# Performance work log

Measured on AMD Instinct MI355X. Metric: run time of the kernel, lower is better.

The kernel has to match this reference:

```python
import jax, jax.numpy as jnp
import numpy as np


def _bucket_ids(x, min_t_idx, sz):
    # torch .long() truncates toward zero; x >= 0 so trunc == floor
    y = (x * sz).astype(jnp.int32)
    NI = x.shape[1]
    mt = min_t_idx.astype(jnp.int32)
    if NI == 2:
        return y[:, 0] * sz + y[:, 1] + mt * sz ** 2
    elif NI == 3:
        return y[:, 0] * sz ** 2 + y[:, 1] * sz + y[:, 2] + mt * sz ** 3
    else:
        raise AssertionError('Only 2D and 3D are supported')


def _max_bucket(x, min_t_idx, K, sz):
    # concrete (numpy) computation of the max bucket occupancy -> pad width M
    xn = np.asarray(x); mt = np.asarray(min_t_idx)
    msk = mt > 0
    y = (xn[msk] * sz).astype(np.int64)
    NI = xn.shape[1]
    if NI == 2:
        yf = y[:, 0] * sz + y[:, 1] + mt[msk].astype(np.int64) * sz ** 2
    else:
        yf = y[:, 0] * sz ** 2 + y[:, 1] * sz + y[:, 2] + mt[msk].astype(np.int64) * sz ** 3
    return max(int(np.bincount(yf).max()), K)


def _forward(x, min_t_idx, K, sz, M):
    N, NI = x.shape
    m = min_t_idx > 0
    y_f = _bucket_ids(x, min_t_idx, sz)
    # inactive points get unique singleton buckets sorted past all real ones
    BIG = jnp.int32(1 << 20)
    y_f = jnp.where(m, y_f, BIG + jnp.arange(N, dtype=jnp.int32))
    order = jnp.argsort(y_f)
    xs = x[order]              # [N, NI] sorted by bucket
    yfs = y_f[order]
    ms = m[order]
    # contiguous bucket extent for every point (block-diagonal ranges)
    left = jnp.searchsorted(yfs, yfs, side='left')
    count = jnp.searchsorted(yfs, yfs, side='right') - left
    # gather up-to-M in-bucket neighbors per point
    nb = jnp.arange(M)
    idx = jnp.clip(left[:, None] + nb[None, :], 0, N - 1)   # [N, M]
    nb_valid = nb[None, :] < count[:, None]                  # [N, M]
    xn = xs[idx]                                             # [N, M, NI]
    d2 = jnp.sum((xs[:, None, :] - xn) ** 2, axis=-1)        # [N, M]
    d2 = jnp.where(nb_valid, d2, jnp.inf)
    # K-th smallest squared distance in bucket (self included, dist 0) == argKmin[:, -1]
    kth = -jax.lax.top_k(-d2, K)[0][:, K - 1]
    w = jnp.sqrt(kth)
    dim = NI - 1
    if dim == 1:
        p_m = w * 2.0 / (K - 1)
    elif dim == 2:
        p_m = (w ** 2) * jnp.pi / (K - 1)
    else:
        p_m = (4.0 / 3.0) * (w ** 3) * jnp.pi / (K - 1)
    p_sorted = jnp.where(ms, p_m, 0.0)
    # scatter back to original ordering (p[m] = p_m[inv_sort_idx])
    return jnp.zeros(N, x.dtype).at[order].set(p_sorted)


def setup_inputs():
    key = jax.random.key(0)
    k1, k2 = jax.random.split(key)
    x = jax.random.uniform(k1, (262144, 3), dtype=jnp.float32)
    min_t_idx = jax.random.randint(k2, (262144,), 0, 32, dtype=jnp.int32)
    return {"x": x, "min_t_idx": min_t_idx, "K": 16, "sz": 5}


def reference(x, min_t_idx, K, sz):
    M = _max_bucket(x, min_t_idx, K, sz)
    return _forward(x, min_t_idx, K, sz, M)
```

## Files before the change

### kernel.cpp

```cpp
#include <hip/hip_runtime.h>
#include <math.h>

#define KK 16
#define NBUCK 4000
#define NBPAD 4096
#define CAP 128
#define INF_F __builtin_inff()

__global__ __launch_bounds__(256) void zero_kernel(int* __restrict__ counts) {
    int i = blockIdx.x * blockDim.x + threadIdx.x;
    if (i < NBPAD) counts[i] = 0;
}

__global__ __launch_bounds__(256) void build_kernel(const float4* __restrict__ xf4,
                                                    const int4* __restrict__ mt4,
                                                    int* __restrict__ counts,
                                                    float4* __restrict__ slab,
                                                    float* __restrict__ out, int N4) {
    int g = blockIdx.x * blockDim.x + threadIdx.x;
    if (g >= N4) return;
    float4 a = xf4[g * 3 + 0];
    float4 b = xf4[g * 3 + 1];
    float4 c = xf4[g * 3 + 2];
    int4 m = mt4[g];
    int i0 = g * 4;
    float px[4] = {a.x, a.w, b.z, c.y};
    float py[4] = {a.y, b.x, b.w, c.z};
    float pz[4] = {a.z, b.y, c.x, c.w};
    int   pm[4] = {m.x, m.y, m.z, m.w};
#pragma unroll
    for (int t = 0; t < 4; ++t) {
        int mm = pm[t];
        if (mm <= 0) { out[i0 + t] = 0.0f; continue; }
        float x0 = px[t], x1 = py[t], x2 = pz[t];
        int bid = mm * 125 + (int)(x0 * 5.0f) * 25 + (int)(x1 * 5.0f) * 5 + (int)(x2 * 5.0f);
        int pos = atomicAdd(&counts[bid], 1);
        if (pos < CAP)
            slab[(bid << 7) + pos] = make_float4(x0, x1, x2, __int_as_float(i0 + t));
    }
}

#define CAS(a, b) { float _lo = fminf(a, b); float _hi = fmaxf(a, b); a = _lo; b = _hi; }

#define SORT16_D \
  CAS(d0,d1) CAS(d2,d3) CAS(d4,d5) CAS(d6,d7) CAS(d8,d9) CAS(d10,d11) CAS(d12,d13) CAS(d14,d15) \
  CAS(d0,d2) CAS(d1,d3) CAS(d4,d6) CAS(d5,d7) CAS(d8,d10) CAS(d9,d11) CAS(d12,d14) CAS(d13,d15) \
  CAS(d1,d2) CAS(d5,d6) CAS(d9,d10) CAS(d13,d14) \
  CAS(d0,d4) CAS(d1,d5) CAS(d2,d6) CAS(d3,d7) CAS(d8,d12) CAS(d9,d13) CAS(d10,d14) CAS(d11,d15) \
  CAS(d2,d4) CAS(d3,d5) CAS(d10,d12) CAS(d11,d13) \
  CAS(d1,d2) CAS(d3,d4) CAS(d5,d6) CAS(d9,d10) CAS(d11,d12) CAS(d13,d14) \
  CAS(d0,d8) CAS(d1,d9) CAS(d2,d10) CAS(d3,d11) CAS(d4,d12) CAS(d5,d13) CAS(d6,d14) CAS(d7,d15) \
  CAS(d4,d8) CAS(d5,d9) CAS(d6,d10) CAS(d7,d11) \
  CAS(d2,d4) CAS(d3,d5) CAS(d6,d8) CAS(d7,d9) CAS(d10,d12) CAS(d11,d13) \
  CAS(d1,d2) CAS(d3,d4) CAS(d5,d6) CAS(d7,d8) CAS(d9,d10) CAS(d11,d12) CAS(d13,d14)

#define LOADD(t) { int j = j0 + (t); int jc = (j < e) ? j : (e - 1); \
    float4 q = slab[jc]; \
    float ax = mex - q.x; float ay = mey - q.y; float az = mez - q.z; \
    float dd = ax * ax + ay * ay + az * az; \
    d##t = (j < e) ? dd : INF_F; }

#define LOADALL \
  LOADD(0) LOADD(1) LOADD(2) LOADD(3) LOADD(4) LOADD(5) LOADD(6) LOADD(7) \
  LOADD(8) LOADD(9) LOADD(10) LOADD(11) LOADD(12) LOADD(13) LOADD(14) LOADD(15)

#define HALFCLEAN \
  t0 = fminf(t0, d15); t1 = fminf(t1, d14); t2 = fminf(t2, d13); t3 = fminf(t3, d12); \
  t4 = fminf(t4, d11); t5 = fminf(t5, d10); t6 = fminf(t6, d9);  t7 = fminf(t7, d8);  \
  t8 = fminf(t8, d7);  t9 = fminf(t9, d6);  t10 = fminf(t10, d5); t11 = fminf(t11, d4); \
  t12 = fminf(t12, d3); t13 = fminf(t13, d2); t14 = fminf(t14, d1); t15 = fminf(t15, d0);

#define MERGE16_T \
  CAS(t0,t8) CAS(t1,t9) CAS(t2,t10) CAS(t3,t11) CAS(t4,t12) CAS(t5,t13) CAS(t6,t14) CAS(t7,t15) \
  CAS(t0,t4) CAS(t1,t5) CAS(t2,t6) CAS(t3,t7) CAS(t8,t12) CAS(t9,t13) CAS(t10,t14) CAS(t11,t15) \
  CAS(t0,t2) CAS(t1,t3) CAS(t4,t6) CAS(t5,t7) CAS(t8,t10) CAS(t9,t11) CAS(t12,t14) CAS(t13,t15) \
  CAS(t0,t1) CAS(t2,t3) CAS(t4,t5) CAS(t6,t7) CAS(t8,t9) CAS(t10,t11) CAS(t12,t13) CAS(t14,t15)

__global__ __launch_bounds__(256, 6) void knn_kernel(const float4* __restrict__ slab,
                                                     const int* __restrict__ counts,
                                                     float* __restrict__ out) {
    int b = blockIdx.x;
    int cnt = counts[b];
    cnt = (cnt > CAP) ? CAP : cnt;
    int tid = threadIdx.x;
    int slot = tid >> 1;
    int slice = tid & 1;
    if (slot >= cnt) return;

    int s = b << 7;
    int e = s + cnt;
    float4 me = slab[s + slot];
    float mex = me.x, mey = me.y, mez = me.z;
    int oidx = __float_as_int(me.w);

    float d0, d1, d2, d3, d4, d5, d6, d7, d8, d9, d10, d11, d12, d13, d14, d15;
    float t0, t1, t2, t3, t4, t5, t6, t7, t8, t9, t10, t11, t12, t13, t14, t15;

    int j0 = s + slice * 16;
    if (j0 < e) {
        LOADALL
        SORT16_D
        t0 = d0;  t1 = d1;  t2 = d2;   t3 = d3;   t4 = d4;   t5 = d5;   t6 = d6;   t7 = d7;
        t8 = d8;  t9 = d9;  t10 = d10; t11 = d11; t12 = d12; t13 = d13; t14 = d14; t15 = d15;
        for (j0 += 32; j0 < e; j0 += 32) {
            LOADALL
            SORT16_D
            HALFCLEAN
            MERGE16_T
        }
    } else {
        t0 = t1 = t2 = t3 = t4 = t5 = t6 = t7 = INF_F;
        t8 = t9 = t10 = t11 = t12 = t13 = t14 = t15 = INF_F;
    }

    float p0  = __shfl_xor(t0, 1),  p1  = __shfl_xor(t1, 1);
    float p2  = __shfl_xor(t2, 1),  p3  = __shfl_xor(t3, 1);
    float p4  = __shfl_xor(t4, 1),  p5  = __shfl_xor(t5, 1);
    float p6  = __shfl_xor(t6, 1),  p7  = __shfl_xor(t7, 1);
    float p8  = __shfl_xor(t8, 1),  p9  = __shfl_xor(t9, 1);
    float p10 = __shfl_xor(t10, 1), p11 = __shfl_xor(t11, 1);
    float p12 = __shfl_xor(t12, 1), p13 = __shfl_xor(t13, 1);
    float p14 = __shfl_xor(t14, 1), p15 = __shfl_xor(t15, 1);

    if (slice == 0) {
        float u0  = fminf(t0,  p15), u1  = fminf(t1,  p14);
        float u2  = fminf(t2,  p13), u3  = fminf(t3,  p12);
        float u4  = fminf(t4,  p11), u5  = fminf(t5,  p10);
        float u6  = fminf(t6,  p9),  u7  = fminf(t7,  p8);
        float u8  = fminf(t8,  p7),  u9  = fminf(t9,  p6);
        float u10 = fminf(t10, p5),  u11 = fminf(t11, p4);
        float u12 = fminf(t12, p3),  u13 = fminf(t13, p2);
        float u14 = fminf(t14, p1),  u15 = fminf(t15, p0);
        float aa = fmaxf(fmaxf(fmaxf(u0, u1), fmaxf(u2, u3)),
                         fmaxf(fmaxf(u4, u5), fmaxf(u6, u7)));
        float bb = fmaxf(fmaxf(fmaxf(u8, u9), fmaxf(u10, u11)),
                         fmaxf(fmaxf(u12, u13), fmaxf(u14, u15)));
        float kth = fmaxf(aa, bb);
        float w = sqrtf(kth);
        out[oidx] = (w * w) * 3.14159265358979323846f / 15.0f;
    }
}

extern "C" void kernel_launch(void* const* d_in, const int* in_sizes, int n_in,
                              void* d_out, int out_size, void* d_ws, size_t ws_size,
                              hipStream_t stream) {
    const float* x  = (const float*)d_in[0];
    const int*   mt = (const int*)d_in[1];
    float* out = (float*)d_out;
    int N = in_sizes[1];

    char* ws = (char*)d_ws;
    int*    counts = (int*)(ws);
    float4* slab   = (float4*)(ws + 65536);

    int N4 = N / 4;
    zero_kernel<<<NBPAD / 256, 256, 0, stream>>>(counts);
    build_kernel<<<(N4 + 255) / 256, 256, 0, stream>>>((const float4*)x, (const int4*)mt,
                                                       counts, slab, out, N4);
    knn_kernel<<<NBUCK, 256, 0, stream>>>(slab, counts, out);
}
```

Baseline: 61.10 us.

## Stage bucket points in shared memory with INF padding; simplify build to one point per thread

The knn kernel now loads each bucket's points once into LDS, padding up to a multiple of 16 with INF coordinates. This removes the per-element bounds clamp and select in the distance loop and serves the repeated reads from shared memory instead of global or L2. The build kernel goes back to one point per thread with scalar loads, in place of the vectorized four-points-per-thread version. That gives more threads and atomics in flight, but the loads are less coalesced. The change also adds a block barrier.

```diff
diff --git a/kernel.cpp b/kernel.cpp
--- a/kernel.cpp
+++ b/kernel.cpp
@@ -12,32 +12,20 @@
     if (i < NBPAD) counts[i] = 0;
 }
 
-__global__ __launch_bounds__(256) void build_kernel(const float4* __restrict__ xf4,
-                                                    const int4* __restrict__ mt4,
+__global__ __launch_bounds__(256) void build_kernel(const float* __restrict__ x,
+                                                    const int* __restrict__ mt,
                                                     int* __restrict__ counts,
                                                     float4* __restrict__ slab,
-                                                    float* __restrict__ out, int N4) {
-    int g = blockIdx.x * blockDim.x + threadIdx.x;
-    if (g >= N4) return;
-    float4 a = xf4[g * 3 + 0];
-    float4 b = xf4[g * 3 + 1];
-    float4 c = xf4[g * 3 + 2];
-    int4 m = mt4[g];
-    int i0 = g * 4;
-    float px[4] = {a.x, a.w, b.z, c.y};
-    float py[4] = {a.y, b.x, b.w, c.z};
-    float pz[4] = {a.z, b.y, c.x, c.w};
-    int   pm[4] = {m.x, m.y, m.z, m.w};
-#pragma unroll
-    for (int t = 0; t < 4; ++t) {
-        int mm = pm[t];
-        if (mm <= 0) { out[i0 + t] = 0.0f; continue; }
-        float x0 = px[t], x1 = py[t], x2 = pz[t];
-        int bid = mm * 125 + (int)(x0 * 5.0f) * 25 + (int)(x1 * 5.0f) * 5 + (int)(x2 * 5.0f);
-        int pos = atomicAdd(&counts[bid], 1);
-        if (pos < CAP)
-            slab[(bid << 7) + pos] = make_float4(x0, x1, x2, __int_as_float(i0 + t));
-    }
+                                                    float* __restrict__ out, int N) {
+    int i = blockIdx.x * blockDim.x + threadIdx.x;
+    if (i >= N) return;
+    int m = mt[i];
+    if (m <= 0) { out[i] = 0.0f; return; }
+    float x0 = x[3 * i], x1 = x[3 * i + 1], x2 = x[3 * i + 2];
+    int bid = m * 125 + (int)(x0 * 5.0f) * 25 + (int)(x1 * 5.0f) * 5 + (int)(x2 * 5.0f);
+    int pos = atomicAdd(&counts[bid], 1);
+    if (pos < CAP)
+        slab[(bid << 7) + pos] = make_float4(x0, x1, x2, __int_as_float(i));
 }
 
 #define CAS(a, b) { float _lo = fminf(a, b); float _hi = fmaxf(a, b); a = _lo; b = _hi; }
@@ -54,11 +42,9 @@
   CAS(d2,d4) CAS(d3,d5) CAS(d6,d8) CAS(d7,d9) CAS(d10,d12) CAS(d11,d13) \
   CAS(d1,d2) CAS(d3,d4) CAS(d5,d6) CAS(d7,d8) CAS(d9,d10) CAS(d11,d12) CAS(d13,d14)
 
-#define LOADD(t) { int j = j0 + (t); int jc = (j < e) ? j : (e - 1); \
-    float4 q = slab[jc]; \
+#define LOADD(t) { float4 q = pts[j0 + (t)]; \
     float ax = mex - q.x; float ay = mey - q.y; float az = mez - q.z; \
-    float dd = ax * ax + ay * ay + az * az; \
-    d##t = (j < e) ? dd : INF_F; }
+    d##t = ax * ax + ay * ay + az * az; }
 
 #define LOADALL \
   LOADD(0) LOADD(1) LOADD(2) LOADD(3) LOADD(4) LOADD(5) LOADD(6) LOADD(7) \
@@ -79,30 +65,38 @@
 __global__ __launch_bounds__(256, 6) void knn_kernel(const float4* __restrict__ slab,
                                                      const int* __restrict__ counts,
                                                      float* __restrict__ out) {
+    __shared__ float4 pts[CAP];
     int b = blockIdx.x;
     int cnt = counts[b];
     cnt = (cnt > CAP) ? CAP : cnt;
+    int cnt_pad = (cnt + 15) & ~15;
     int tid = threadIdx.x;
+
+    if (tid < cnt) {
+        pts[tid] = slab[(b << 7) + tid];
+    } else if (tid < cnt_pad) {
+        pts[tid] = make_float4(INF_F, INF_F, INF_F, 0.0f);
+    }
+    __syncthreads();
+
     int slot = tid >> 1;
     int slice = tid & 1;
     if (slot >= cnt) return;
 
-    int s = b << 7;
-    int e = s + cnt;
-    float4 me = slab[s + slot];
+    float4 me = pts[slot];
     float mex = me.x, mey = me.y, mez = me.z;
     int oidx = __float_as_int(me.w);
 
     float d0, d1, d2, d3, d4, d5, d6, d7, d8, d9, d10, d11, d12, d13, d14, d15;
     float t0, t1, t2, t3, t4, t5, t6, t7, t8, t9, t10, t11, t12, t13, t14, t15;
 
-    int j0 = s + slice * 16;
-    if (j0 < e) {
+    int j0 = slice * 16;
+    if (j0 < cnt_pad) {
         LOADALL
         SORT16_D
         t0 = d0;  t1 = d1;  t2 = d2;   t3 = d3;   t4 = d4;   t5 = d5;   t6 = d6;   t7 = d7;
         t8 = d8;  t9 = d9;  t10 = d10; t11 = d11; t12 = d12; t13 = d13; t14 = d14; t15 = d15;
-        for (j0 += 32; j0 < e; j0 += 32) {
+        for (j0 += 32; j0 < cnt_pad; j0 += 32) {
             LOADALL
             SORT16_D
             HALFCLEAN
@@ -153,9 +147,7 @@
     int*    counts = (int*)(ws);
     float4* slab   = (float4*)(ws + 65536);
 
-    int N4 = N / 4;
     zero_kernel<<<NBPAD / 256, 256, 0, stream>>>(counts);
-    build_kernel<<<(N4 + 255) / 256, 256, 0, stream>>>((const float4*)x, (const int4*)mt,
-                                                       counts, slab, out, N4);
+    build_kernel<<<(N + 255) / 256, 256, 0, stream>>>(x, mt, counts, slab, out, N);
     knn_kernel<<<NBUCK, 256, 0, stream>>>(slab, counts, out);
 }
```

After: 54.55 us (median of 2 runs). -10.7%, faster.
